# Kernel optimization log

Hardware: AMD Instinct MI355X
Metric: run time of the kernel (lower is better)

## Reference

```python
import jax, jax.numpy as jnp
import numpy as np

NODES_PER_GRAPH = 32
NUM_GRAPHS = 4096
N = NUM_GRAPHS * NODES_PER_GRAPH  # 131072
DEG = 8
E = N * DEG
FEAT = 10


def setup_inputs() -> dict:
    key = jax.random.key(0)
    ks = jax.random.split(key, 32)
    x = jax.random.normal(ks[0], (N, FEAT), dtype=jnp.float32)
    src = jnp.repeat(jnp.arange(N, dtype=jnp.int64), DEG)
    dst = (src // NODES_PER_GRAPH) * NODES_PER_GRAPH + jax.random.randint(
        ks[1], (E,), 0, NODES_PER_GRAPH).astype(jnp.int64)
    edge_index = jnp.stack([src, dst])  # [2, E], row0 = source j, row1 = target i
    batch = (jnp.arange(N, dtype=jnp.int64) // NODES_PER_GRAPH)

    def lin(k, fan_in, shape):
        return jax.random.normal(k, shape, dtype=jnp.float32) / np.sqrt(fan_in)

    inp = dict(x=x, edge_index=edge_index, batch=batch)
    inp['Wq'] = lin(ks[2], 32, (32, 32))
    inp['Wk'] = lin(ks[3], 32, (32, 32))
    inp['Wv'] = lin(ks[4], 32, (32, 32))
    inp['W1'] = lin(ks[5], 10, (10, 64));  inp['a1s'] = lin(ks[6], 16, (4, 16))
    inp['a1d'] = lin(ks[7], 16, (4, 16));  inp['b1'] = jnp.zeros((64,), jnp.float32)
    inp['W2'] = lin(ks[8], 64, (64, 64));  inp['a2s'] = lin(ks[9], 16, (4, 16))
    inp['a2d'] = lin(ks[10], 16, (4, 16)); inp['b2'] = jnp.zeros((64,), jnp.float32)
    inp['W3'] = lin(ks[11], 64, (64, 64)); inp['a3s'] = lin(ks[12], 16, (4, 16))
    inp['a3d'] = lin(ks[13], 16, (4, 16)); inp['b3'] = jnp.zeros((64,), jnp.float32)
    inp['W4'] = lin(ks[14], 64, (64, 64)); inp['a4s'] = lin(ks[15], 64, (1, 64))
    inp['a4d'] = lin(ks[16], 64, (1, 64)); inp['b4'] = jnp.zeros((64,), jnp.float32)
    inp['fcW'] = lin(ks[17], 64, (64, 2)); inp['fcb'] = jnp.zeros((2,), jnp.float32)
    return inp


def gat_conv(x, src, dst, W, a_s, a_d, b, heads, out_c, concat):
    n = x.shape[0]
    h = (x @ W).reshape(n, heads, out_c)                    # [N,H,C]
    e_s = jnp.einsum('nhc,hc->nh', h, a_s)
    e_d = jnp.einsum('nhc,hc->nh', h, a_d)
    e = jax.nn.leaky_relu(e_s[src] + e_d[dst], 0.2)          # [E,H]
    e_max = jax.ops.segment_max(e, dst, num_segments=n)
    e = jnp.exp(e - e_max[dst])
    denom = jax.ops.segment_sum(e, dst, num_segments=n)
    alpha = e / (denom[dst] + 1e-16)                         # softmax per target node
    msg = h[src] * alpha[:, :, None]                         # [E,H,C]
    out = jax.ops.segment_sum(msg, dst, num_segments=n)      # [N,H,C]
    out = out.reshape(n, heads * out_c) if concat else out.mean(axis=1)
    return out + b


def forward(x, edge_index, batch, Wq, Wk, Wv, W1, a1s, a1d, b1, W2, a2s, a2d, b2,
            W3, a3s, a3d, b3, W4, a4s, a4d, b4, fcW, fcb):
    n = x.shape[0]
    b = n // NODES_PER_GRAPH
    # Attention_Layer1: (b*32, 10) -> (b, 10, 32)
    att_in = x.reshape(b, NODES_PER_GRAPH, FEAT).transpose(0, 2, 1)  # [b, sl=10, 32]
    Q = att_in @ Wq
    K = att_in @ Wk
    V = att_in @ Wv
    alpha = jax.nn.softmax(jnp.einsum('bsi,bti->bst', Q, K), axis=2)
    out = jnp.einsum('bst,bti->bsi', alpha, V)               # [b, 10, 32]
    # rearrange 'b i sl -> (b sl) i' with i=10, sl=32
    xg = out.transpose(0, 2, 1).reshape(n, FEAT)             # [(b*32), 10]
    # add self-loops (PyG GATConv default)
    loops = jnp.arange(n, dtype=edge_index.dtype)
    src = jnp.concatenate([edge_index[0], loops])
    dst = jnp.concatenate([edge_index[1], loops])
    xg = jax.nn.leaky_relu(gat_conv(xg, src, dst, W1, a1s, a1d, b1, 4, 16, True), 0.01)
    xg = jax.nn.leaky_relu(gat_conv(xg, src, dst, W2, a2s, a2d, b2, 4, 16, True), 0.01)
    xg = jax.nn.leaky_relu(gat_conv(xg, src, dst, W3, a3s, a3d, b3, 4, 16, True), 0.01)
    xg = jax.nn.leaky_relu(gat_conv(xg, src, dst, W4, a4s, a4d, b4, 1, 64, True), 0.01)
    # global mean pool per graph
    sums = jax.ops.segment_sum(xg, batch, num_segments=b)
    cnts = jax.ops.segment_sum(jnp.ones((n, 1), xg.dtype), batch, num_segments=b)
    pooled = sums / cnts                                     # [b, 64]
    logits = pooled @ fcW + fcb                              # [b, 2]
    probas = jax.nn.softmax(logits, axis=1)
    return logits, probas


def reference(x, edge_index, batch, Wq, Wk, Wv, W1, a1s, a1d, b1, W2, a2s, a2d, b2,
              W3, a3s, a3d, b3, W4, a4s, a4d, b4, fcW, fcb):
    return forward(x, edge_index, batch, Wq, Wk, Wv, W1, a1s, a1d, b1, W2, a2s, a2d,
                   b2, W3, a3s, a3d, b3, W4, a4s, a4d, b4, fcW, fcb)
```

## Files before the change

### kernel.cpp

```cpp
#include <hip/hip_runtime.h>


#define NGRAPH 4096
#define EDGES  (NGRAPH * 256)
#define NT     256
#define XS     68
#define LOG2E  1.4426950408889634f

typedef __attribute__((ext_vector_type(8))) short bf16x8;
typedef __attribute__((ext_vector_type(4))) float f32x4;
typedef __attribute__((ext_vector_type(4))) int   i32x4;

__device__ __forceinline__ unsigned f2u(float x){ union{float f;unsigned u;}c;c.f=x;return c.u; }
__device__ __forceinline__ float u2f(unsigned u){ union{unsigned u;float f;}c;c.u=u;return c.f; }

__device__ __forceinline__ void split2(float x0, float x1, unsigned& dhi, unsigned& dlo){
    const unsigned u0 = f2u(x0), u1 = f2u(x1);
    dhi = (u0 >> 16) | (u1 & 0xffff0000u);
    const float l0 = x0 - u2f(u0 & 0xffff0000u);
    const float l1 = x1 - u2f(u1 & 0xffff0000u);
    dlo = (f2u(l0) >> 16) | (f2u(l1) & 0xffff0000u);
}

__device__ __forceinline__ f32x4 mfma16(i32x4 a, i32x4 b, f32x4 c){
    return __builtin_amdgcn_mfma_f32_16x16x32_bf16(
        __builtin_bit_cast(bf16x8, a), __builtin_bit_cast(bf16x8, b), c, 0, 0, 0);
}

template<int KSTEPS>
__device__ __forceinline__ void gat_layer(
    int tid, float (*xa)[XS], unsigned* hTw, float* esw, float* edw,
    const unsigned char* A8, const char* __restrict__ ws, int l,
    const float* __restrict__ b_g)
{
    const int lane = tid & 63, w = tid >> 6;
    const int n15 = lane & 15, q = lane >> 4;

    {
        const int row = lane & 31, half = lane >> 5;
        const float* wasp = (const float*)(ws + 65536 + (l*4+w)*256) + half*32;
        const float* wadp = (const float*)(ws + 69632 + (l*4+w)*256) + half*32;
        const float* xr = &xa[row][half*32];
        float es = 0.f, ed = 0.f;
#pragma unroll
        for (int k4 = 0; k4 < 32; k4 += 4){
            const float4 xv = *(const float4*)&xr[k4];
            const float4 sv = __ldg((const float4*)&wasp[k4]);
            const float4 dv = __ldg((const float4*)&wadp[k4]);
            es += xv.x*sv.x + xv.y*sv.y + xv.z*sv.z + xv.w*sv.w;
            ed += xv.x*dv.x + xv.y*dv.y + xv.z*dv.z + xv.w*dv.w;
        }
        es += __shfl_xor(es, 32);
        ed += __shfl_xor(ed, 32);
        if (half == 0) esw[row] = es; else edw[row] = ed;
    }

    f32x4 hC0 = {0,0,0,0}, hC1 = {0,0,0,0};
#pragma unroll
    for (int ks = 0; ks < KSTEPS; ++ks){
        const unsigned short* wr = (const unsigned short*)(ws + l*16384)
                                   + (w*16 + n15)*64 + ks*32 + q*8;
        const i32x4 bh = *(const i32x4*)wr;
        const i32x4 bl = *(const i32x4*)(wr + 4096);
#pragma unroll
        for (int mt = 0; mt < 2; ++mt){
            const float* ar = &xa[mt*16 + n15][ks*32 + q*8];
            const float4 a0 = *(const float4*)ar;
            const float4 a1 = *(const float4*)(ar + 4);
            i32x4 ah, al; unsigned th, tl;
            split2(a0.x, a0.y, th, tl); ah[0] = (int)th; al[0] = (int)tl;
            split2(a0.z, a0.w, th, tl); ah[1] = (int)th; al[1] = (int)tl;
            split2(a1.x, a1.y, th, tl); ah[2] = (int)th; al[2] = (int)tl;
            split2(a1.z, a1.w, th, tl); ah[3] = (int)th; al[3] = (int)tl;
            f32x4 acc = mt ? hC1 : hC0;
            acc = mfma16(ah, bh, acc);
            acc = mfma16(ah, bl, acc);
            acc = mfma16(al, bh, acc);
            if (mt) hC1 = acc; else hC0 = acc;
        }
    }
    __syncthreads();

#pragma unroll
    for (int mt = 0; mt < 2; ++mt){
        const f32x4 hv = mt ? hC1 : hC0;
#pragma unroll
        for (int r = 0; r < 4; ++r){
            const float xv = hv[r];
            const unsigned u = f2u(xv);
            const float lo = xv - u2f(u & 0xffff0000u);
            hTw[n15*37 + mt*16 + q*4 + r] = (u >> 16) | (f2u(lo) & 0xffff0000u);
        }
    }

    float pf0[8], pf1[8];
    float ss0 = 0.f, ss1 = 0.f;
    {
        float es8[8];
        *(float4*)&es8[0] = *(const float4*)&esw[q*8];
        *(float4*)&es8[4] = *(const float4*)&esw[q*8 + 4];
        const float ed0 = edw[n15], ed1 = edw[16 + n15];
        const uint2 c0 = *(const uint2*)&A8[n15*40 + q*8];
        const uint2 c1 = *(const uint2*)&A8[(16 + n15)*40 + q*8];
#pragma unroll
        for (int jj = 0; jj < 8; ++jj){
            const unsigned cnt0 = ((jj < 4 ? c0.x >> (8*jj) : c0.y >> (8*(jj-4))) & 0xffu);
            const unsigned cnt1 = ((jj < 4 ? c1.x >> (8*jj) : c1.y >> (8*(jj-4))) & 0xffu);
            float e0 = es8[jj] + ed0; e0 = fmaxf(e0, 0.2f*e0);
            float e1 = es8[jj] + ed1; e1 = fmaxf(e1, 0.2f*e1);
            const float p0 = (float)cnt0 * exp2f(e0);
            const float p1 = (float)cnt1 * exp2f(e1);
            pf0[jj] = p0; ss0 += p0;
            pf1[jj] = p1; ss1 += p1;
        }
        ss0 += __shfl_xor(ss0, 16); ss0 += __shfl_xor(ss0, 32);
        ss1 += __shfl_xor(ss1, 16); ss1 += __shfl_xor(ss1, 32);
        if (q == 0){
            edw[n15]      = 1.f/(ss0 + 1e-16f);
            edw[16 + n15] = 1.f/(ss1 + 1e-16f);
        }
    }

    {
        unsigned hd[8];
#pragma unroll
        for (int jj = 0; jj < 8; ++jj) hd[jj] = hTw[n15*37 + q*8 + jj];
        i32x4 bh, bl;
#pragma unroll
        for (int r = 0; r < 4; ++r){
            bh[r] = (int)((hd[2*r] & 0xffffu) | (hd[2*r+1] << 16));
            bl[r] = (int)((hd[2*r] >> 16)    | (hd[2*r+1] & 0xffff0000u));
        }
        f32x4 o0 = {0,0,0,0}, o1 = {0,0,0,0};
        i32x4 ph, pl; unsigned th, tl;
#pragma unroll
        for (int r = 0; r < 4; ++r){
            split2(pf0[2*r], pf0[2*r+1], th, tl); ph[r] = (int)th; pl[r] = (int)tl;
        }
        o0 = mfma16(ph, bh, o0); o0 = mfma16(ph, bl, o0); o0 = mfma16(pl, bh, o0);
#pragma unroll
        for (int r = 0; r < 4; ++r){
            split2(pf1[2*r], pf1[2*r+1], th, tl); ph[r] = (int)th; pl[r] = (int)tl;
        }
        o1 = mfma16(ph, bh, o1); o1 = mfma16(ph, bl, o1); o1 = mfma16(pl, bh, o1);

        const float bv = __ldg(b_g + w*16 + n15);
#pragma unroll
        for (int mt = 0; mt < 2; ++mt){
            const f32x4 ov = mt ? o1 : o0;
#pragma unroll
            for (int r = 0; r < 4; ++r){
                const int row = mt*16 + q*4 + r;
                float v = ov[r] * edw[row] + bv;
                v = fmaxf(v, 0.01f*v);
                xa[row][w*16 + n15] = v;
            }
        }
    }
}

__global__ __launch_bounds__(NT) void gnn_fused(
    const float* __restrict__ x, const int* __restrict__ edge_index,
    const float* __restrict__ Wq, const float* __restrict__ Wk, const float* __restrict__ Wv,
    const float* __restrict__ b1, const float* __restrict__ b2,
    const float* __restrict__ b3, const float* __restrict__ b4,
    const float* __restrict__ fcW, const float* __restrict__ fcb,
    const char* __restrict__ ws, float* __restrict__ out)
{
    __shared__ __align__(16) float xa[32][XS];
    __shared__ __align__(16) unsigned hTp[4][592];
    __shared__ __align__(16) float es_l[4][32];
    __shared__ __align__(16) float ed_l[4][32];
    __shared__ __align__(16) unsigned char A8[32*40];

    const int g = blockIdx.x, tid = threadIdx.x;
    const int w = tid >> 6;
    int* A32 = (int*)&xa[0][0];
    float* scr = (float*)&hTp[0][0];
    float* xin = scr;
    float* qkv = scr + 384;
    float* sc  = scr + 1374;

    for (int idx = tid; idx < 1024; idx += NT) A32[idx] = 0;
    for (int idx = tid; idx < 320; idx += NT)
        xin[(idx/10)*12 + (idx%10)] = x[g*320 + idx];
    __syncthreads();

    {
        const int* dstp = edge_index + EDGES + g*256;
        atomicAdd(&A32[(dstp[tid] & 31)*32 + (tid >> 3)], 1);
        if (tid < 32) atomicAdd(&A32[tid*33], 1);
    }
    for (int idx = tid; idx < 960; idx += NT){
        const int mat = idx/320, r = idx - mat*320, s = r >> 5, i = r & 31;
        const float* Wsrc = (mat == 0) ? Wq : ((mat == 1) ? Wk : Wv);
        float acc = 0.f;
#pragma unroll
        for (int mm = 0; mm < 32; ++mm) acc += xin[mm*12 + s]*__ldg(Wsrc + mm*32 + i);
        qkv[mat*330 + s*33 + i] = acc;
    }
    __syncthreads();

    if (tid < 100){
        const int s = tid/10, t = tid - 10*(tid/10);
        const float* qs = qkv + s*33;
        const float* kt = qkv + 330 + t*33;
        float acc = 0.f;
#pragma unroll
        for (int i2 = 0; i2 < 32; ++i2) acc += qs[i2]*kt[i2];
        sc[s*11 + t] = acc;
    }
    __syncthreads();

    {
        const int i = tid >> 3, j4 = (tid & 7)*4;
        const int4 v = *(const int4*)&A32[i*32 + j4];
        *(unsigned*)&A8[i*40 + j4] =
            (unsigned)v.x | ((unsigned)v.y << 8) | ((unsigned)v.z << 16) | ((unsigned)v.w << 24);
    }
    if (tid < 10){
        float* row = sc + tid*11;
        float m = row[0];
#pragma unroll
        for (int t = 1; t < 10; ++t) m = fmaxf(m, row[t]);
        float ssum = 0.f;
#pragma unroll
        for (int t = 0; t < 10; ++t){ const float e = __expf(row[t]-m); row[t] = e; ssum += e; }
        const float inv = 1.f/ssum;
#pragma unroll
        for (int t = 0; t < 10; ++t) row[t] *= inv;
    }
    __syncthreads();

    for (int idx = tid; idx < 2048; idx += NT){
        const int i = idx >> 6, s = idx & 63;
        float acc = 0.f;
        if (s < 10){
#pragma unroll
            for (int t = 0; t < 10; ++t) acc += sc[s*11 + t]*qkv[660 + t*33 + i];
        }
        xa[i][s] = acc;
    }
    __syncthreads();

    unsigned* hTw = hTp[w];
    float* esw = es_l[w];
    float* edw = ed_l[w];
    gat_layer<1>(tid, xa, hTw, esw, edw, A8, ws, 0, b1);
    __syncthreads();
    gat_layer<2>(tid, xa, hTw, esw, edw, A8, ws, 1, b2);
    __syncthreads();
    gat_layer<2>(tid, xa, hTw, esw, edw, A8, ws, 2, b3);
    __syncthreads();
    gat_layer<2>(tid, xa, hTw, esw, edw, A8, ws, 3, b4);
    __syncthreads();

    if (tid < 64){
        float acc = 0.f;
#pragma unroll
        for (int n = 0; n < 32; ++n) acc += xa[n][tid];
        const float p = acc*(1.f/32.f);
        float c0 = p*__ldg(fcW + 2*tid);
        float c1 = p*__ldg(fcW + 2*tid + 1);
#pragma unroll
        for (int off = 32; off > 0; off >>= 1){
            c0 += __shfl_down(c0, off);
            c1 += __shfl_down(c1, off);
        }
        if (tid == 0){
            const float l0 = c0 + __ldg(fcb), l1 = c1 + __ldg(fcb + 1);
            const float m = fmaxf(l0, l1);
            const float e0 = __expf(l0 - m), e1 = __expf(l1 - m);
            const float inv = 1.f/(e0 + e1);
            out[2*g] = l0;
            out[2*g + 1] = l1;
            out[2*NGRAPH + 2*g] = e0*inv;
            out[2*NGRAPH + 2*g + 1] = e1*inv;
        }
    }
}

__global__ void prep(
    const float* __restrict__ W1, const float* __restrict__ W2,
    const float* __restrict__ W3, const float* __restrict__ W4,
    const float* __restrict__ a1s, const float* __restrict__ a1d,
    const float* __restrict__ a2s, const float* __restrict__ a2d,
    const float* __restrict__ a3s, const float* __restrict__ a3d,
    const float* __restrict__ a4s, const float* __restrict__ a4d,
    char* __restrict__ ws)
{
    const int b = blockIdx.x, tid = threadIdx.x;
    const float* Wl[4] = {W1, W2, W3, W4};
    const int Kl[4] = {10, 64, 64, 64};
    if (b < 32){
        const int l = b >> 3;
        const float* W = Wl[l];
        const int K = Kl[l];
        unsigned short* hi = (unsigned short*)(ws + l*16384);
        unsigned short* lo = hi + 4096;
        const int base = (b & 7)*512;
        for (int idx = base + tid; idx < base + 512; idx += NT){
            const int n = idx >> 6, k = idx & 63;
            const float v = (k < K) ? __ldg(W + k*64 + n) : 0.f;
            const unsigned u = f2u(v);
            const float lof = v - u2f(u & 0xffff0000u);
            hi[idx] = (unsigned short)(u >> 16);
            lo[idx] = (unsigned short)(f2u(lof) >> 16);
        }
    } else {
        const int l = b - 32;
        const float* W = Wl[l];
        const int K = Kl[l];
        const float* asp[4] = {a1s, a2s, a3s, a4s};
        const float* adp[4] = {a1d, a2d, a3d, a4d};
        const int hh = tid >> 6, k = tid & 63;
        const int C = (l < 3) ? 16 : 64;
        const int hh_e = (l < 3) ? hh : 0;
        float s = 0.f, d = 0.f;
        if (k < K){
            for (int c = 0; c < C; ++c){
                const float wv = __ldg(W + k*64 + hh_e*C + c);
                s += wv*__ldg(asp[l] + hh_e*C + c);
                d += wv*__ldg(adp[l] + hh_e*C + c);
            }
        }
        ((float*)(ws + 65536 + (l*4 + hh)*256))[k] = s*LOG2E;
        ((float*)(ws + 69632 + (l*4 + hh)*256))[k] = d*LOG2E;
    }
}

extern "C" void kernel_launch(void* const* d_in, const int* in_sizes, int n_in,
                              void* d_out, int out_size, void* d_ws, size_t ws_size,
                              hipStream_t stream) {
    (void)in_sizes; (void)n_in; (void)ws_size; (void)out_size;
    prep<<<36, NT, 0, stream>>>(
        (const float*)d_in[6], (const float*)d_in[10], (const float*)d_in[14], (const float*)d_in[18],
        (const float*)d_in[7], (const float*)d_in[8],
        (const float*)d_in[11], (const float*)d_in[12],
        (const float*)d_in[15], (const float*)d_in[16],
        (const float*)d_in[19], (const float*)d_in[20],
        (char*)d_ws);
    gnn_fused<<<NGRAPH, NT, 0, stream>>>(
        (const float*)d_in[0], (const int*)d_in[1],
        (const float*)d_in[3], (const float*)d_in[4], (const float*)d_in[5],
        (const float*)d_in[9], (const float*)d_in[13], (const float*)d_in[17], (const float*)d_in[21],
        (const float*)d_in[22], (const float*)d_in[23],
        (const char*)d_ws, (float*)d_out);
}
```

Before: 218.2 us.

## Store activations as pre-split bf16 hi/lo and compute attention logits via MFMA

Activations in shared memory now live as separate bf16 hi and lo planes instead of fp32, so the per-layer fp32-to-bf16 split before the MFMA is gone and A operands load directly as vectors. The source and destination attention scores are folded into an extra MFMA tile with pre-split weights, prepared in the prep kernel, replacing the scalar dot-product loop. The h transpose buffer is also stored as split planes, which removes the repacking before the aggregation MFMA. In exchange, the split now happens once at each layer output, each layer issues extra MFMAs for a mostly zero score tile, and the prep kernel writes a larger workspace region.

```diff
diff --git a/kernel.cpp b/kernel.cpp
--- a/kernel.cpp
+++ b/kernel.cpp
@@ -4,7 +4,6 @@
 #define NGRAPH 4096
 #define EDGES  (NGRAPH * 256)
 #define NT     256
-#define XS     68
 #define LOG2E  1.4426950408889634f
 
 typedef __attribute__((ext_vector_type(8))) short bf16x8;
@@ -29,57 +28,47 @@
 
 template<int KSTEPS>
 __device__ __forceinline__ void gat_layer(
-    int tid, float (*xa)[XS], unsigned* hTw, float* esw, float* edw,
+    int tid, unsigned short (*xh)[72], unsigned short (*xl)[72],
+    unsigned short* hh_w, unsigned short* hl_w, float* esw, float* edw,
     const unsigned char* A8, const char* __restrict__ ws, int l,
     const float* __restrict__ b_g)
 {
     const int lane = tid & 63, w = tid >> 6;
     const int n15 = lane & 15, q = lane >> 4;
 
-    {
-        const int row = lane & 31, half = lane >> 5;
-        const float* wasp = (const float*)(ws + 65536 + (l*4+w)*256) + half*32;
-        const float* wadp = (const float*)(ws + 69632 + (l*4+w)*256) + half*32;
-        const float* xr = &xa[row][half*32];
-        float es = 0.f, ed = 0.f;
-#pragma unroll
-        for (int k4 = 0; k4 < 32; k4 += 4){
-            const float4 xv = *(const float4*)&xr[k4];
-            const float4 sv = __ldg((const float4*)&wasp[k4]);
-            const float4 dv = __ldg((const float4*)&wadp[k4]);
-            es += xv.x*sv.x + xv.y*sv.y + xv.z*sv.z + xv.w*sv.w;
-            ed += xv.x*dv.x + xv.y*dv.y + xv.z*dv.z + xv.w*dv.w;
-        }
-        es += __shfl_xor(es, 32);
-        ed += __shfl_xor(ed, 32);
-        if (half == 0) esw[row] = es; else edw[row] = ed;
-    }
-
     f32x4 hC0 = {0,0,0,0}, hC1 = {0,0,0,0};
+    f32x4 eC0 = {0,0,0,0}, eC1 = {0,0,0,0};
 #pragma unroll
     for (int ks = 0; ks < KSTEPS; ++ks){
         const unsigned short* wr = (const unsigned short*)(ws + l*16384)
                                    + (w*16 + n15)*64 + ks*32 + q*8;
         const i32x4 bh = *(const i32x4*)wr;
         const i32x4 bl = *(const i32x4*)(wr + 4096);
-#pragma unroll
-        for (int mt = 0; mt < 2; ++mt){
-            const float* ar = &xa[mt*16 + n15][ks*32 + q*8];
-            const float4 a0 = *(const float4*)ar;
-            const float4 a1 = *(const float4*)(ar + 4);
-            i32x4 ah, al; unsigned th, tl;
-            split2(a0.x, a0.y, th, tl); ah[0] = (int)th; al[0] = (int)tl;
-            split2(a0.z, a0.w, th, tl); ah[1] = (int)th; al[1] = (int)tl;
-            split2(a1.x, a1.y, th, tl); ah[2] = (int)th; al[2] = (int)tl;
-            split2(a1.z, a1.w, th, tl); ah[3] = (int)th; al[3] = (int)tl;
-            f32x4 acc = mt ? hC1 : hC0;
-            acc = mfma16(ah, bh, acc);
-            acc = mfma16(ah, bl, acc);
-            acc = mfma16(al, bh, acc);
-            if (mt) hC1 = acc; else hC0 = acc;
-        }
-    }
-    __syncthreads();
+        const unsigned short* er = (const unsigned short*)(ws + 65536)
+                                   + (l*4 + w)*2048 + n15*64 + ks*32 + q*8;
+        const i32x4 eh = *(const i32x4*)er;
+        const i32x4 el = *(const i32x4*)(er + 1024);
+
+        const i32x4 a0h = *(const i32x4*)&xh[n15][ks*32 + q*8];
+        const i32x4 a0l = *(const i32x4*)&xl[n15][ks*32 + q*8];
+        hC0 = mfma16(a0h, bh, hC0); hC0 = mfma16(a0h, bl, hC0); hC0 = mfma16(a0l, bh, hC0);
+        eC0 = mfma16(a0h, eh, eC0); eC0 = mfma16(a0h, el, eC0); eC0 = mfma16(a0l, eh, eC0);
+
+        const i32x4 a1h = *(const i32x4*)&xh[16 + n15][ks*32 + q*8];
+        const i32x4 a1l = *(const i32x4*)&xl[16 + n15][ks*32 + q*8];
+        hC1 = mfma16(a1h, bh, hC1); hC1 = mfma16(a1h, bl, hC1); hC1 = mfma16(a1l, bh, hC1);
+        eC1 = mfma16(a1h, eh, eC1); eC1 = mfma16(a1h, el, eC1); eC1 = mfma16(a1l, eh, eC1);
+    }
+    __syncthreads();
+
+    if (n15 < 2){
+        float* dst = n15 ? edw : esw;
+#pragma unroll
+        for (int r = 0; r < 4; ++r){
+            dst[q*4 + r]      = eC0[r];
+            dst[16 + q*4 + r] = eC1[r];
+        }
+    }
 
 #pragma unroll
     for (int mt = 0; mt < 2; ++mt){
@@ -89,12 +78,12 @@
             const float xv = hv[r];
             const unsigned u = f2u(xv);
             const float lo = xv - u2f(u & 0xffff0000u);
-            hTw[n15*37 + mt*16 + q*4 + r] = (u >> 16) | (f2u(lo) & 0xffff0000u);
+            hh_w[n15*40 + mt*16 + q*4 + r] = (unsigned short)(u >> 16);
+            hl_w[n15*40 + mt*16 + q*4 + r] = (unsigned short)(f2u(lo) >> 16);
         }
     }
 
     float pf0[8], pf1[8];
-    float ss0 = 0.f, ss1 = 0.f;
     {
         float es8[8];
         *(float4*)&es8[0] = *(const float4*)&esw[q*8];
@@ -102,6 +91,7 @@
         const float ed0 = edw[n15], ed1 = edw[16 + n15];
         const uint2 c0 = *(const uint2*)&A8[n15*40 + q*8];
         const uint2 c1 = *(const uint2*)&A8[(16 + n15)*40 + q*8];
+        float ss0 = 0.f, ss1 = 0.f;
 #pragma unroll
         for (int jj = 0; jj < 8; ++jj){
             const unsigned cnt0 = ((jj < 4 ? c0.x >> (8*jj) : c0.y >> (8*(jj-4))) & 0xffu);
@@ -122,15 +112,8 @@
     }
 
     {
-        unsigned hd[8];
-#pragma unroll
-        for (int jj = 0; jj < 8; ++jj) hd[jj] = hTw[n15*37 + q*8 + jj];
-        i32x4 bh, bl;
-#pragma unroll
-        for (int r = 0; r < 4; ++r){
-            bh[r] = (int)((hd[2*r] & 0xffffu) | (hd[2*r+1] << 16));
-            bl[r] = (int)((hd[2*r] >> 16)    | (hd[2*r+1] & 0xffff0000u));
-        }
+        const i32x4 bh = *(const i32x4*)&hh_w[n15*40 + q*8];
+        const i32x4 bl = *(const i32x4*)&hl_w[n15*40 + q*8];
         f32x4 o0 = {0,0,0,0}, o1 = {0,0,0,0};
         i32x4 ph, pl; unsigned th, tl;
 #pragma unroll
@@ -153,7 +136,10 @@
                 const int row = mt*16 + q*4 + r;
                 float v = ov[r] * edw[row] + bv;
                 v = fmaxf(v, 0.01f*v);
-                xa[row][w*16 + n15] = v;
+                const unsigned u = f2u(v);
+                const float lo = v - u2f(u & 0xffff0000u);
+                xh[row][w*16 + n15] = (unsigned short)(u >> 16);
+                xl[row][w*16 + n15] = (unsigned short)(f2u(lo) >> 16);
             }
         }
     }
@@ -167,16 +153,16 @@
     const float* __restrict__ fcW, const float* __restrict__ fcb,
     const char* __restrict__ ws, float* __restrict__ out)
 {
-    __shared__ __align__(16) float xa[32][XS];
-    __shared__ __align__(16) unsigned hTp[4][592];
+    __shared__ __align__(16) unsigned short xap[2][32][72];
+    __shared__ __align__(16) unsigned short hT[4][2][16][40];
     __shared__ __align__(16) float es_l[4][32];
     __shared__ __align__(16) float ed_l[4][32];
     __shared__ __align__(16) unsigned char A8[32*40];
 
     const int g = blockIdx.x, tid = threadIdx.x;
     const int w = tid >> 6;
-    int* A32 = (int*)&xa[0][0];
-    float* scr = (float*)&hTp[0][0];
+    int* A32 = (int*)&xap[0][0][0];
+    float* scr = (float*)&hT[0][0][0][0];
     float* xin = scr;
     float* qkv = scr + 384;
     float* sc  = scr + 1374;
@@ -239,26 +225,33 @@
 #pragma unroll
             for (int t = 0; t < 10; ++t) acc += sc[s*11 + t]*qkv[660 + t*33 + i];
         }
-        xa[i][s] = acc;
-    }
-    __syncthreads();
-
-    unsigned* hTw = hTp[w];
+        const unsigned u = f2u(acc);
+        const float lo = acc - u2f(u & 0xffff0000u);
+        xap[0][i][s] = (unsigned short)(u >> 16);
+        xap[1][i][s] = (unsigned short)(f2u(lo) >> 16);
+    }
+    __syncthreads();
+
+    unsigned short (*xh)[72] = xap[0];
+    unsigned short (*xl)[72] = xap[1];
+    unsigned short* hh_w = &hT[w][0][0][0];
+    unsigned short* hl_w = &hT[w][1][0][0];
     float* esw = es_l[w];
     float* edw = ed_l[w];
-    gat_layer<1>(tid, xa, hTw, esw, edw, A8, ws, 0, b1);
-    __syncthreads();
-    gat_layer<2>(tid, xa, hTw, esw, edw, A8, ws, 1, b2);
-    __syncthreads();
-    gat_layer<2>(tid, xa, hTw, esw, edw, A8, ws, 2, b3);
-    __syncthreads();
-    gat_layer<2>(tid, xa, hTw, esw, edw, A8, ws, 3, b4);
+    gat_layer<1>(tid, xh, xl, hh_w, hl_w, esw, edw, A8, ws, 0, b1);
+    __syncthreads();
+    gat_layer<2>(tid, xh, xl, hh_w, hl_w, esw, edw, A8, ws, 1, b2);
+    __syncthreads();
+    gat_layer<2>(tid, xh, xl, hh_w, hl_w, esw, edw, A8, ws, 2, b3);
+    __syncthreads();
+    gat_layer<2>(tid, xh, xl, hh_w, hl_w, esw, edw, A8, ws, 3, b4);
     __syncthreads();
 
     if (tid < 64){
         float acc = 0.f;
 #pragma unroll
-        for (int n = 0; n < 32; ++n) acc += xa[n][tid];
+        for (int n = 0; n < 32; ++n)
+            acc += u2f(((unsigned)xap[0][n][tid]) << 16) + u2f(((unsigned)xap[1][n][tid]) << 16);
         const float p = acc*(1.f/32.f);
         float c0 = p*__ldg(fcW + 2*tid);
         float c1 = p*__ldg(fcW + 2*tid + 1);
@@ -313,19 +306,24 @@
         const int K = Kl[l];
         const float* asp[4] = {a1s, a2s, a3s, a4s};
         const float* adp[4] = {a1d, a2d, a3d, a4d};
-        const int hh = tid >> 6, k = tid & 63;
         const int C = (l < 3) ? 16 : 64;
-        const int hh_e = (l < 3) ? hh : 0;
-        float s = 0.f, d = 0.f;
-        if (k < K){
-            for (int c = 0; c < C; ++c){
-                const float wv = __ldg(W + k*64 + hh_e*C + c);
-                s += wv*__ldg(asp[l] + hh_e*C + c);
-                d += wv*__ldg(adp[l] + hh_e*C + c);
+        unsigned short* base = (unsigned short*)(ws + 65536);
+        for (int idx = tid; idx < 4096; idx += NT){
+            const int wv = idx >> 10, rem = idx & 1023, n = rem >> 6, k = rem & 63;
+            float val = 0.f;
+            if (n < 2 && k < K){
+                const int hh = (l < 3) ? wv : 0;
+                const float* av = n ? adp[l] : asp[l];
+                float s = 0.f;
+                for (int c = 0; c < C; ++c)
+                    s += __ldg(W + k*64 + hh*C + c) * __ldg(av + hh*C + c);
+                val = s * LOG2E;
             }
-        }
-        ((float*)(ws + 65536 + (l*4 + hh)*256))[k] = s*LOG2E;
-        ((float*)(ws + 69632 + (l*4 + hh)*256))[k] = d*LOG2E;
+            const unsigned u = f2u(val);
+            const float lof = val - u2f(u & 0xffff0000u);
+            base[(l*4 + wv)*2048 + n*64 + k] = (unsigned short)(u >> 16);
+            base[(l*4 + wv)*2048 + 1024 + n*64 + k] = (unsigned short)(f2u(lof) >> 16);
+        }
     }
 }
 
```

Result: slower. 226.3 us (+3.7%).
